# Optimization experiments

Measured on AMD Instinct MI355X. Metric: run time of the kernel, lower is better.

The kernel has to match this reference:

```python
import jax, jax.numpy as jnp
import numpy as np
from jax import lax

B, H, W = 64, 40, 40
K = 24        # num_capsules == num_templates
TS = 11       # template_size
F = 16        # num_feature_maps
PI = 3.141592653589793


def setup_inputs() -> dict:
    key = jax.random.key(0)
    ks = jax.random.split(key, 12)
    def nrm(k, shape, s):
        return jax.random.normal(k, shape, dtype=jnp.float32) * s
    inp = {"x": jax.random.normal(ks[0], (B, 1, H, W), dtype=jnp.float32)}
    wshapes = [(K, 128, 1, 3, 3), (K, 128, 128, 3, 3), (K, 128, 128, 3, 3), (K, 128, 128, 3, 3), (K, F, 128, 1, 1)]
    for i, sh in enumerate(wshapes):
        fan_in = sh[2] * sh[3] * sh[4]
        inp["w%d" % (i + 1)] = nrm(ks[1 + i], sh, (2.0 / fan_in) ** 0.5)
        inp["b%d" % (i + 1)] = nrm(ks[6 + i], (K, sh[1]), 0.1)
    inp["templates"] = jax.random.normal(ks[11], (K, TS, TS), dtype=jnp.float32)
    return inp


def _capsule(x, w1, b1, w2, b2, w3, b3, w4, b4, w5, b5):
    # one part-capsule conv stack; x: [B,1,H,W]
    def cv(h, w, b, s):
        y = lax.conv_general_dilated(h, w, (s, s), 'VALID', dimension_numbers=('NCHW', 'OIHW', 'NCHW'))
        return y + b[None, :, None, None]
    h = jax.nn.relu(cv(x, w1, b1, 2))
    h = jax.nn.relu(cv(h, w2, b2, 2))
    h = jax.nn.relu(cv(h, w3, b3, 1))
    h = jax.nn.relu(cv(h, w4, b4, 1))
    return cv(h, w5, b5, 1)  # [B,F,5,5]


def _warp(templates, pose, Ho, Wo):
    # Batched replacement for the per-sample PIL affine + resize round-trip.
    # templates: [T,TS,TS]; pose: [B,T,6] = (angle_deg, tx, ty, scale, shear_x_deg, shear_y_deg)
    T_ = templates.shape[0]
    ang = jnp.deg2rad(pose[..., 0])
    tx, ty = pose[..., 1], pose[..., 2]
    sc = jnp.maximum(pose[..., 3], 1e-2)  # guard against scale==0 from ReLU
    shx = jnp.deg2rad(pose[..., 4])
    shy = jnp.deg2rad(pose[..., 5])
    cx = cy = (TS - 1) * 0.5
    # torchvision _get_inverse_affine_matrix
    a = jnp.cos(ang - shy) / jnp.cos(shy)
    b = -jnp.cos(ang - shy) * jnp.tan(shx) / jnp.cos(shy) - jnp.sin(ang)
    c = jnp.sin(ang - shy) / jnp.cos(shy)
    d = -jnp.sin(ang - shy) * jnp.tan(shx) / jnp.cos(shy) + jnp.cos(ang)
    m0 = d / sc; m1 = -b / sc; m3 = -c / sc; m4 = a / sc
    m2 = m0 * (-cx - tx) + m1 * (-cy - ty) + cx
    m5 = m3 * (-cx - tx) + m4 * (-cy - ty) + cy
    # output grid in template pixel coords (fuses the bilinear resize TS->HoxWo)
    gy = (jnp.arange(Ho, dtype=jnp.float32) + 0.5) * TS / Ho - 0.5
    gx = (jnp.arange(Wo, dtype=jnp.float32) + 0.5) * TS / Wo - 0.5
    yo, xo = jnp.meshgrid(gy, gx, indexing='ij')  # [Ho,Wo]
    xin = m0[..., None, None] * xo + m1[..., None, None] * yo + m2[..., None, None]  # [B,T,Ho,Wo]
    yin = m3[..., None, None] * xo + m4[..., None, None] * yo + m5[..., None, None]
    x0 = jnp.floor(xin); y0 = jnp.floor(yin)
    wx = xin - x0; wy = yin - y0
    x0i = x0.astype(jnp.int32); y0i = y0.astype(jnp.int32)
    tidx = jnp.arange(T_)[None, :, None, None]
    def tap(yi, xi):
        valid = (xi >= 0) & (xi < TS) & (yi >= 0) & (yi < TS)
        v = templates[tidx, jnp.clip(yi, 0, TS - 1), jnp.clip(xi, 0, TS - 1)]
        return jnp.where(valid, v, 0.0)
    return (tap(y0i, x0i) * (1 - wx) * (1 - wy) + tap(y0i, x0i + 1) * wx * (1 - wy)
            + tap(y0i + 1, x0i) * (1 - wx) * wy + tap(y0i + 1, x0i + 1) * wx * wy)


def reference(x, w1, b1, w2, b2, w3, b3, w4, b4, w5, b5, templates):
    out = jax.vmap(_capsule, in_axes=(None,) + (0,) * 10)(x, w1, b1, w2, b2, w3, b3, w4, b4, w5, b5)  # [K,B,F,5,5]
    # torch Softmax(2) on [B,Hc,Wc] attention map = softmax over each row (last axis)
    att = jax.nn.softmax(out[:, :, -1], axis=-1)                       # [K,B,5,5]
    pooled = jnp.sum(out[:, :, :-1] * att[:, :, None], axis=(-2, -1))  # [K,B,F-1]
    p = pooled.transpose(1, 0, 2)                                      # [B,K,F-1]
    x_m = jax.nn.relu(p[:, :, :6])
    d_m = jax.nn.sigmoid(p[:, :, 6:7])
    c_z = jax.nn.relu(p[:, :, 7:])
    Bn = x.shape[0]
    # PIL round-trip in the original detaches gradients from templates/poses
    tt = lax.stop_gradient(_warp(templates, x_m, H, W))                # [B,K,H,W]
    mix = jax.nn.softmax(d_m * tt.reshape(Bn, K, -1), axis=-1).reshape(Bn, K, H, W)
    std = jnp.std(x.reshape(Bn, -1), axis=-1, ddof=1).reshape(Bn, 1, 1, 1)
    mult = 1.0 / jnp.sqrt(std * 2.0 * PI)
    pw = -1.0 / (2.0 * std * std)
    g = mult * jnp.exp((lax.stop_gradient(x) - tt) ** 2 * pw)          # [B,K,H,W]
    ll = jnp.mean(jnp.sum(jnp.log(jnp.sum(g * mix, axis=1)), axis=(-2, -1)))
    tflat = jnp.broadcast_to(lax.stop_gradient(templates).reshape(1, K, TS * TS), (Bn, K, TS * TS))
    input_ocae = jnp.concatenate([lax.stop_gradient(d_m), lax.stop_gradient(x_m), tflat, c_z], axis=-1)
    return ll, input_ocae, lax.stop_gradient(x_m), lax.stop_gradient(d_m)
```

## Files before the change

### kernel.cpp

```cpp
#include <hip/hip_runtime.h>
#include <math.h>

#define TPB 256

typedef __attribute__((ext_vector_type(8))) short s16x8;
typedef __attribute__((ext_vector_type(4))) short s16x4;
typedef __attribute__((ext_vector_type(4))) float f32x4;
typedef unsigned int u32;

constexpr int Bn = 64, Kc = 24, TSz = 11;
constexpr int NBK = Bn * Kc;
constexpr int P2 = 81, P3 = 49, P4 = 25;

constexpr size_t SZW_B    = (size_t)Kc * 36 * 4096 * 2;
constexpr size_t OFFB_W2  = 0;
constexpr size_t OFFB_W3  = OFFB_W2 + SZW_B;
constexpr size_t OFFB_W4  = OFFB_W3 + SZW_B;
constexpr size_t OFFB_POSE= OFFB_W4 + SZW_B;
constexpr size_t OFFB_DMV = OFFB_POSE + (size_t)NBK * 6 * 4;
constexpr size_t OFFB_TT  = OFFB_DMV + (size_t)NBK * 4;
constexpr size_t OFFB_ST  = OFFB_TT + (size_t)NBK * 1600 * 4;
constexpr size_t OFFB_MXS = OFFB_ST + 512;
constexpr size_t OFFB_PART= OFFB_MXS + (size_t)NBK * 2 * 4;

constexpr int OUT_OC = 1;
constexpr int OUT_XM = 1 + NBK * 136;
constexpr int OUT_DM = OUT_XM + NBK * 6;

__device__ __forceinline__ ushort f2b(float f) {
    union { float f; unsigned u; } c; c.f = f;
    unsigned r = c.u + 0x7fffu + ((c.u >> 16) & 1u);
    return (ushort)(r >> 16);
}
__device__ __forceinline__ float b2f(ushort h) {
    union { unsigned u; float f; } c; c.u = ((unsigned)h) << 16; return c.f;
}

__device__ __forceinline__ float blockReduceSum(float v) {
    __shared__ float red[4];
    __syncthreads();
#pragma unroll
    for (int o = 32; o > 0; o >>= 1) v += __shfl_down(v, o, 64);
    int lane = threadIdx.x & 63, wv = threadIdx.x >> 6;
    if (lane == 0) red[wv] = v;
    __syncthreads();
    return red[0] + red[1] + red[2] + red[3];
}

__device__ __forceinline__ float blockReduceMax(float v) {
    __shared__ float redm[4];
    __syncthreads();
#pragma unroll
    for (int o = 32; o > 0; o >>= 1) v = fmaxf(v, __shfl_down(v, o, 64));
    int lane = threadIdx.x & 63, wv = threadIdx.x >> 6;
    if (lane == 0) redm[wv] = v;
    __syncthreads();
    return fmaxf(fmaxf(redm[0], redm[1]), fmaxf(redm[2], redm[3]));
}

__global__ __launch_bounds__(TPB) void prep_k(
    const float* __restrict__ w2, const float* __restrict__ w3,
    const float* __restrict__ w4, const float* __restrict__ x,
    ushort* __restrict__ wt2, ushort* __restrict__ wt3,
    ushort* __restrict__ wt4, float* __restrict__ st) {
    const int bid = blockIdx.x;
    if (bid < 9216) {
        __shared__ float ld[1152];
        const float* w = bid < 3072 ? w2 : (bid < 6144 ? w3 : w4);
        ushort* wt = bid < 3072 ? wt2 : (bid < 6144 ? wt3 : wt4);
        const int kb = bid & 3071;
        const int kk = (bid % 3072) >> 7, cout = bid & 127;
        (void)kb;
        const float* src = w + (size_t)(kk * 128 + cout) * 1152;
        for (int i = threadIdx.x; i < 1152; i += TPB) ld[i] = src[i];
        __syncthreads();
        const int n = cout >> 4, l16 = cout & 15;
        for (int e = threadIdx.x; e < 1152; e += TPB) {
            int cb = e / 288, r = e - cb * 288, tap = r >> 5, c32 = r & 31;
            int cin = cb * 32 + c32;
            size_t d = (size_t)((kk * 4 + cb) * 9 + tap) * 4096
                     + n * 512 + (c32 >> 3) * 128 + l16 * 8 + (c32 & 7);
            wt[d] = f2b(ld[cin * 9 + tap]);
        }
    } else {
        const int b = bid - 9216;
        const float* xb = x + b * 1600;
        float s = 0.f, s2 = 0.f;
        for (int p = threadIdx.x; p < 1600; p += TPB) {
            float v = xb[p];
            s += v; s2 += v * v;
        }
        s = blockReduceSum(s);
        s2 = blockReduceSum(s2);
        if (threadIdx.x == 0) {
            float mean = s / 1600.f;
            float var = (s2 - 1600.f * mean * mean) / 1599.f;
            float sd = sqrtf(var);
            st[b * 2] = rsqrtf(sd * 6.283185307179586f);
            st[b * 2 + 1] = -1.f / (2.f * sd * sd);
        }
    }
}

__global__ __launch_bounds__(256) void convall_k(
    const float* __restrict__ x, const float* __restrict__ w1,
    const float* __restrict__ b1,
    const ushort* __restrict__ wt2, const float* __restrict__ b2,
    const ushort* __restrict__ wt3, const float* __restrict__ b3,
    const ushort* __restrict__ wt4, const float* __restrict__ b4,
    const float* __restrict__ w5, const float* __restrict__ b5,
    const float* __restrict__ tpl,
    float* __restrict__ pose, float* __restrict__ dmv,
    float* __restrict__ out) {
    __shared__ __align__(16) ushort pool[17680];
    float*  xs  = (float*)pool;
    ushort* As  = pool + 3200;
    ushort* h2L = pool;
    ushort* h3L = pool + 11016;
    float*  h4s = (float*)pool;
    float*  outs= (float*)(pool + 6400);
    float*  atts= (float*)(pool + 7200);
    float*  pooled = (float*)(pool + 7264);

    const int bi = blockIdx.x;
    const int xcd = bi & 7, jj = bi >> 3;
    const int k = xcd * 3 + jj % 3, b = jj / 3;
    const int bkL = b * 24 + k;
    const int tid = threadIdx.x;
    const int w = tid >> 6, l = tid & 63, l16 = l & 15, g = l >> 4;
    const int mgrp = w >> 1, ngrp = w & 1;

    {
        constexpr int OP = 81, STR = 40;
        const int sl = tid & 7, p0 = tid >> 3;
        const ushort* wb = wt2 + (size_t)k * 36 * 4096 + ngrp * 2048 + g * 128 + l16 * 8;
        const float* w1k = w1 + (size_t)k * 1152;
        const float* b1k = b1 + k * 128;

        for (int i = tid; i < 400; i += 256)
            ((f32x4*)xs)[i] = ((const f32x4*)(x + b * 1600))[i];

        s16x8 breg[3][4];
#pragma unroll
        for (int n = 0; n < 4; ++n) breg[0][n] = *(const s16x8*)(wb + n * 512);
#pragma unroll
        for (int n = 0; n < 4; ++n) breg[1][n] = *(const s16x8*)(wb + 4096 + n * 512);

        f32x4 acc[3][4];
#pragma unroll
        for (int m = 0; m < 3; ++m)
#pragma unroll
            for (int n = 0; n < 4; ++n) acc[m][n] = (f32x4)0.f;

        int ibase[3];
#pragma unroll
        for (int m = 0; m < 3; ++m) {
            int row = (mgrp * 3 + m) * 16 + l16;
            row = row < OP ? row : OP - 1;
            int oy = row / 9, ox = row - oy * 9;
            ibase[m] = oy * 38 + ox * 2;
        }

        float wq[36], bq[4];
        auto conv1_slab = [&]() {
            for (int p = p0; p < 361; p += 32) {
                int py = p / 19, px = p - py * 19;
                const float* xb = xs + py * 80 + px * 2;
                float xt[9];
#pragma unroll
                for (int dy = 0; dy < 3; ++dy)
#pragma unroll
                    for (int dx = 0; dx < 3; ++dx) xt[dy * 3 + dx] = xb[dy * 40 + dx];
                s16x4 v;
#pragma unroll
                for (int j2 = 0; j2 < 4; ++j2) {
                    float s2 = bq[j2];
#pragma unroll
                    for (int t9 = 0; t9 < 9; ++t9) s2 += wq[j2 * 9 + t9] * xt[t9];
                    v[j2] = (short)f2b(fmaxf(s2, 0.f));
                }
                *(s16x4*)(As + p * STR + 8 * ((sl >> 1) ^ ((p >> 3) & 1)) + (sl & 1) * 4) = v;
            }
        };

        {
            const float* wsrc = w1k + (sl * 4) * 9;
#pragma unroll
            for (int i2 = 0; i2 < 9; ++i2) ((f32x4*)wq)[i2] = ((const f32x4*)wsrc)[i2];
            *(f32x4*)bq = *(const f32x4*)(b1k + sl * 4);
        }
        __syncthreads();
        conv1_slab();
        __syncthreads();

#pragma unroll
        for (int cb = 0; cb < 4; ++cb) {
            if (cb < 3) {
                const float* wsrc = w1k + ((cb + 1) * 32 + sl * 4) * 9;
#pragma unroll
                for (int i2 = 0; i2 < 9; ++i2) ((f32x4*)wq)[i2] = ((const f32x4*)wsrc)[i2];
                *(f32x4*)bq = *(const f32x4*)(b1k + (cb + 1) * 32 + sl * 4);
            }
#pragma unroll
            for (int tap = 0; tap < 9; ++tap) {
                const int it = cb * 9 + tap;
                if (it + 2 < 36) {
                    const ushort* src = wb + (size_t)(it + 2) * 4096;
#pragma unroll
                    for (int n = 0; n < 4; ++n)
                        breg[(it + 2) % 3][n] = *(const s16x8*)(src + n * 512);
                }
                const int ioff = (tap / 3) * 19 + (tap % 3);
                s16x8 a[3];
#pragma unroll
                for (int m = 0; m < 3; ++m) {
                    int ip = ibase[m] + ioff;
                    a[m] = *(const s16x8*)(As + ip * STR + 8 * (g ^ ((ip >> 3) & 1)));
                }
#pragma unroll
                for (int n = 0; n < 4; ++n)
#pragma unroll
                    for (int m = 0; m < 3; ++m)
                        acc[m][n] = __builtin_amdgcn_mfma_f32_16x16x32_bf16(a[m], breg[it % 3][n], acc[m][n], 0, 0, 0);
            }
            if (cb < 3) {
                __syncthreads();
                conv1_slab();
                __syncthreads();
            }
        }
        __syncthreads();
#pragma unroll
        for (int n = 0; n < 4; ++n) {
            int cout = (ngrp * 4 + n) * 16 + l16;
            float bv = b2[k * 128 + cout];
#pragma unroll
            for (int m = 0; m < 3; ++m)
#pragma unroll
                for (int r = 0; r < 4; ++r) {
                    int row = (mgrp * 3 + m) * 16 + g * 4 + r;
                    if (row < OP)
                        h2L[row * 136 + cout] = f2b(fmaxf(acc[m][n][r] + bv, 0.f));
                }
        }
    }
    __syncthreads();

    {
        constexpr int OP = 49;
        const ushort* wb = wt3 + (size_t)k * 36 * 4096 + ngrp * 2048 + g * 128 + l16 * 8;
        s16x8 breg[2][4];
#pragma unroll
        for (int n = 0; n < 4; ++n) breg[0][n] = *(const s16x8*)(wb + n * 512);
#pragma unroll
        for (int n = 0; n < 4; ++n) breg[1][n] = *(const s16x8*)(wb + 4096 + n * 512);

        f32x4 acc[2][4];
#pragma unroll
        for (int m = 0; m < 2; ++m)
#pragma unroll
            for (int n = 0; n < 4; ++n) acc[m][n] = (f32x4)0.f;

        int ibase[2];
#pragma unroll
        for (int m = 0; m < 2; ++m) {
            int row = (mgrp * 2 + m) * 16 + l16;
            row = row < OP ? row : OP - 1;
            int oy = row / 7, ox = row - oy * 7;
            ibase[m] = oy * 9 + ox;
        }
#pragma unroll
        for (int cb = 0; cb < 4; ++cb)
#pragma unroll
            for (int tap = 0; tap < 9; ++tap) {
                const int it = cb * 9 + tap;
                if (it + 1 < 36) {
                    const ushort* src = wb + (size_t)(it + 1) * 4096;
#pragma unroll
                    for (int n = 0; n < 4; ++n)
                        breg[(it + 1) & 1][n] = *(const s16x8*)(src + n * 512);
                }
                const int ioff = (tap / 3) * 9 + (tap % 3);
                s16x8 a[2];
#pragma unroll
                for (int m = 0; m < 2; ++m)
                    a[m] = *(const s16x8*)(h2L + (ibase[m] + ioff) * 136 + cb * 32 + g * 8);
#pragma unroll
                for (int n = 0; n < 4; ++n)
#pragma unroll
                    for (int m = 0; m < 2; ++m)
                        acc[m][n] = __builtin_amdgcn_mfma_f32_16x16x32_bf16(a[m], breg[it & 1][n], acc[m][n], 0, 0, 0);
            }
#pragma unroll
        for (int n = 0; n < 4; ++n) {
            int cout = (ngrp * 4 + n) * 16 + l16;
            float bv = b3[k * 128 + cout];
#pragma unroll
            for (int m = 0; m < 2; ++m)
#pragma unroll
                for (int r = 0; r < 4; ++r) {
                    int row = (mgrp * 2 + m) * 16 + g * 4 + r;
                    if (row < OP)
                        h3L[row * 136 + cout] = f2b(fmaxf(acc[m][n][r] + bv, 0.f));
                }
        }
    }
    __syncthreads();

    {
        constexpr int OP = 25;
        const ushort* wb = wt4 + (size_t)k * 36 * 4096 + ngrp * 2048 + g * 128 + l16 * 8;
        s16x8 breg[2][4];
#pragma unroll
        for (int n = 0; n < 4; ++n) breg[0][n] = *(const s16x8*)(wb + n * 512);
#pragma unroll
        for (int n = 0; n < 4; ++n) breg[1][n] = *(const s16x8*)(wb + 4096 + n * 512);

        f32x4 acc[4];
#pragma unroll
        for (int n = 0; n < 4; ++n) acc[n] = (f32x4)0.f;

        int ibase;
        {
            int row = mgrp * 16 + l16;
            row = row < OP ? row : OP - 1;
            int oy = row / 5, ox = row - oy * 5;
            ibase = oy * 7 + ox;
        }
#pragma unroll
        for (int cb = 0; cb < 4; ++cb)
#pragma unroll
            for (int tap = 0; tap < 9; ++tap) {
                const int it = cb * 9 + tap;
                if (it + 1 < 36) {
                    const ushort* src = wb + (size_t)(it + 1) * 4096;
#pragma unroll
                    for (int n = 0; n < 4; ++n)
                        breg[(it + 1) & 1][n] = *(const s16x8*)(src + n * 512);
                }
                const int ioff = (tap / 3) * 7 + (tap % 3);
                s16x8 a = *(const s16x8*)(h3L + (ibase + ioff) * 136 + cb * 32 + g * 8);
#pragma unroll
                for (int n = 0; n < 4; ++n)
                    acc[n] = __builtin_amdgcn_mfma_f32_16x16x32_bf16(a, breg[it & 1][n], acc[n], 0, 0, 0);
            }
#pragma unroll
        for (int n = 0; n < 4; ++n) {
            int cout = (ngrp * 4 + n) * 16 + l16;
            float bv = b4[k * 128 + cout];
#pragma unroll
            for (int r = 0; r < 4; ++r) {
                int row = mgrp * 16 + g * 4 + r;
                if (row < OP)
                    h4s[cout * 25 + row] = fmaxf(acc[n][r] + bv, 0.f);
            }
        }
    }
    __syncthreads();

    for (int t = tid; t < 400; t += 256) {
        int f = t / 25, pix = t - f * 25;
        const float* wp = w5 + (size_t)(k * 16 + f) * 128;
        float s = b5[k * 16 + f];
        for (int c = 0; c < 128; ++c) s += wp[c] * h4s[c * 25 + pix];
        outs[t] = s;
    }
    __syncthreads();
    if (tid < 25) {
        int y5 = tid / 5;
        const float* row = outs + 15 * 25 + y5 * 5;
        float mx = row[0];
#pragma unroll
        for (int j = 1; j < 5; ++j) mx = fmaxf(mx, row[j]);
        float ssum = 0.f;
#pragma unroll
        for (int j = 0; j < 5; ++j) ssum += expf(row[j] - mx);
        atts[tid] = expf(outs[15 * 25 + tid] - mx) / ssum;
    }
    __syncthreads();
    if (tid < 15) {
        float s = 0.f;
        const float* row = outs + tid * 25;
#pragma unroll
        for (int p = 0; p < 25; ++p) s += row[p] * atts[p];
        pooled[tid] = s;
    }
    __syncthreads();
    float* oc = out + OUT_OC + (size_t)bkL * 136;
    if (tid < 6) {
        float v = fmaxf(pooled[tid], 0.f);
        pose[bkL * 6 + tid] = v;
        oc[1 + tid] = v;
        out[OUT_XM + bkL * 6 + tid] = v;
    } else if (tid == 6) {
        float d = 1.f / (1.f + expf(-pooled[6]));
        dmv[bkL] = d;
        oc[0] = d;
        out[OUT_DM + bkL] = d;
    } else if (tid >= 7 && tid < 15) {
        oc[128 + tid - 7] = fmaxf(pooled[tid], 0.f);
    }
    for (int t = tid; t < 121; t += 256) oc[7 + t] = tpl[k * 121 + t];
}

__device__ __forceinline__ float tapf(const float* tp, int y, int x) {
    bool valid = (x >= 0) && (x < TSz) && (y >= 0) && (y < TSz);
    int yc = min(max(y, 0), TSz - 1), xc = min(max(x, 0), TSz - 1);
    float v = tp[yc * TSz + xc];
    return valid ? v : 0.f;
}

__global__ __launch_bounds__(TPB) void warp_mix_k(const float* __restrict__ pose,
                                                  const float* __restrict__ tpl,
                                                  const float* __restrict__ dmv,
                                                  float* __restrict__ tt,
                                                  float* __restrict__ mxs) {
    __shared__ float tp[121];
    const int bk = blockIdx.x, k = bk % Kc;
    for (int i = threadIdx.x; i < 121; i += TPB) tp[i] = tpl[k * 121 + i];
    const float* ps = pose + bk * 6;
    const float D2R = 0.017453292519943295f;
    float ang = ps[0] * D2R, tx = ps[1], ty = ps[2];
    float sc = fmaxf(ps[3], 1e-2f);
    float shx = ps[4] * D2R, shy = ps[5] * D2R;
    float cams = cosf(ang - shy), sams = sinf(ang - shy);
    float cshy = cosf(shy), tshx = tanf(shx);
    float av = cams / cshy;
    float bv = -cams * tshx / cshy - sinf(ang);
    float cv = sams / cshy;
    float dv = -sams * tshx / cshy + cosf(ang);
    float m0 = dv / sc, m1 = -bv / sc, m3 = -cv / sc, m4 = av / sc;
    float m2 = m0 * (-5.f - tx) + m1 * (-5.f - ty) + 5.f;
    float m5 = m3 * (-5.f - tx) + m4 * (-5.f - ty) + 5.f;
    __syncthreads();
    float* to = tt + (size_t)bk * 1600;
    float tvl[7];
#pragma unroll
    for (int r = 0; r < 7; ++r) {
        int p = threadIdx.x + r * TPB;
        float val = 0.f;
        if (p < 1600) {
            int i = p / 40, jx = p - (p / 40) * 40;
            float gx = (jx + 0.5f) * (11.f / 40.f) - 0.5f;
            float gy = (i + 0.5f) * (11.f / 40.f) - 0.5f;
            float xin = m0 * gx + m1 * gy + m2;
            float yin = m3 * gx + m4 * gy + m5;
            float x0 = floorf(xin), y0 = floorf(yin);
            float wx = xin - x0, wy = yin - y0;
            int x0i = (int)x0, y0i = (int)y0;
            float v00 = tapf(tp, y0i, x0i),     v01 = tapf(tp, y0i, x0i + 1);
            float v10 = tapf(tp, y0i + 1, x0i), v11 = tapf(tp, y0i + 1, x0i + 1);
            val = v00 * (1.f - wx) * (1.f - wy) + v01 * wx * (1.f - wy) +
                  v10 * (1.f - wx) * wy + v11 * wx * wy;
            to[p] = val;
        }
        tvl[r] = val;
    }
    const float dm = dmv[bk];
    float mx = -1e30f;
#pragma unroll
    for (int r = 0; r < 7; ++r) {
        int p = threadIdx.x + r * TPB;
        if (p < 1600) mx = fmaxf(mx, dm * tvl[r]);
    }
    mx = blockReduceMax(mx);
    float s = 0.f;
#pragma unroll
    for (int r = 0; r < 7; ++r) {
        int p = threadIdx.x + r * TPB;
        if (p < 1600) s += expf(dm * tvl[r] - mx);
    }
    s = blockReduceSum(s);
    if (threadIdx.x == 0) { mxs[bk * 2] = mx; mxs[bk * 2 + 1] = s; }
}

__global__ __launch_bounds__(TPB) void ll_k(const float* __restrict__ x,
                                            const float* __restrict__ tt,
                                            const float* __restrict__ dmv,
                                            const float* __restrict__ mxs,
                                            const float* __restrict__ st,
                                            float* __restrict__ part) {
    const int b = blockIdx.x, sp = blockIdx.y;
    __shared__ float dms[24], mxh[24], sih[24];
    if (threadIdx.x < 24) {
        int bk = b * 24 + threadIdx.x;
        dms[threadIdx.x] = dmv[bk];
        mxh[threadIdx.x] = mxs[bk * 2];
        sih[threadIdx.x] = 1.f / mxs[bk * 2 + 1];
    }
    __syncthreads();
    const float mult = st[b * 2], pw = st[b * 2 + 1];
    const float* xb = x + b * 1600;
    const float* tb = tt + (size_t)b * 24 * 1600;
    float acc = 0.f;
    int p = sp * 200 + threadIdx.x;
    if (threadIdx.x < 200) {
        float xv = xb[p];
        float ssum = 0.f;
        for (int k = 0; k < 24; ++k) {
            float tv = tb[(size_t)k * 1600 + p];
            float dd = xv - tv;
            float g = mult * expf(dd * dd * pw);
            float mixv = expf(dms[k] * tv - mxh[k]) * sih[k];
            ssum += g * mixv;
        }
        acc = logf(ssum);
    }
    acc = blockReduceSum(acc);
    if (threadIdx.x == 0) part[b * 8 + sp] = acc;
}

__global__ void fin_k(const float* __restrict__ part, float* __restrict__ out) {
    float v = 0.f;
#pragma unroll
    for (int q = 0; q < 8; ++q) v += part[threadIdx.x * 8 + q];
#pragma unroll
    for (int o = 32; o > 0; o >>= 1) v += __shfl_down(v, o, 64);
    if (threadIdx.x == 0) out[0] = v * (1.f / 64.f);
}

extern "C" void kernel_launch(void* const* d_in, const int* in_sizes, int n_in,
                              void* d_out, int out_size, void* d_ws, size_t ws_size,
                              hipStream_t stream) {
    const float* x   = (const float*)d_in[0];
    const float* w1  = (const float*)d_in[1];
    const float* b1  = (const float*)d_in[2];
    const float* w2  = (const float*)d_in[3];
    const float* b2  = (const float*)d_in[4];
    const float* w3  = (const float*)d_in[5];
    const float* b3  = (const float*)d_in[6];
    const float* w4  = (const float*)d_in[7];
    const float* b4  = (const float*)d_in[8];
    const float* w5  = (const float*)d_in[9];
    const float* b5  = (const float*)d_in[10];
    const float* tpl = (const float*)d_in[11];
    float* out = (float*)d_out;
    char* W = (char*)d_ws;

    ushort* wt2 = (ushort*)(W + OFFB_W2);
    ushort* wt3 = (ushort*)(W + OFFB_W3);
    ushort* wt4 = (ushort*)(W + OFFB_W4);
    float*  pose = (float*)(W + OFFB_POSE);
    float*  dmv  = (float*)(W + OFFB_DMV);
    float*  ttb  = (float*)(W + OFFB_TT);
    float*  stv  = (float*)(W + OFFB_ST);
    float*  mxs  = (float*)(W + OFFB_MXS);
    float*  part = (float*)(W + OFFB_PART);

    prep_k<<<3 * 3072 + Bn, TPB, 0, stream>>>(w2, w3, w4, x, wt2, wt3, wt4, stv);
    convall_k<<<NBK, 256, 0, stream>>>(x, w1, b1, wt2, b2, wt3, b3, wt4, b4,
                                       w5, b5, tpl, pose, dmv, out);
    warp_mix_k<<<NBK, TPB, 0, stream>>>(pose, tpl, dmv, ttb, mxs);
    ll_k<<<dim3(Bn, 8), TPB, 0, stream>>>(x, ttb, dmv, mxs, stv, part);
    fin_k<<<1, 64, 0, stream>>>(part, out);
}
```

Before: 203.5 us.

## Fuse template warp and softmax stats into conv kernel; shrink weight prefetch ring

Moves the affine template warp and the per-(b,k) softmax max/sum reduction into the tail of the conv kernel, computing pose directly from pooled values in shared memory. This removes one kernel launch and the pose buffer round trip through global memory. It also reduces the bf16 weight register prefetch from triple to double buffering and loads conv1 weights inside the slab lambda. The cost is a longer conv kernel tail and possibly less latency hiding for weight loads.

After: 204.6 us. No clear change (+0.5%).

```diff
diff --git a/kernel.cpp b/kernel.cpp
--- a/kernel.cpp
+++ b/kernel.cpp
@@ -10,14 +10,12 @@
 
 constexpr int Bn = 64, Kc = 24, TSz = 11;
 constexpr int NBK = Bn * Kc;
-constexpr int P2 = 81, P3 = 49, P4 = 25;
 
 constexpr size_t SZW_B    = (size_t)Kc * 36 * 4096 * 2;
 constexpr size_t OFFB_W2  = 0;
 constexpr size_t OFFB_W3  = OFFB_W2 + SZW_B;
 constexpr size_t OFFB_W4  = OFFB_W3 + SZW_B;
-constexpr size_t OFFB_POSE= OFFB_W4 + SZW_B;
-constexpr size_t OFFB_DMV = OFFB_POSE + (size_t)NBK * 6 * 4;
+constexpr size_t OFFB_DMV = OFFB_W4 + SZW_B;
 constexpr size_t OFFB_TT  = OFFB_DMV + (size_t)NBK * 4;
 constexpr size_t OFFB_ST  = OFFB_TT + (size_t)NBK * 1600 * 4;
 constexpr size_t OFFB_MXS = OFFB_ST + 512;
@@ -68,9 +66,7 @@
         __shared__ float ld[1152];
         const float* w = bid < 3072 ? w2 : (bid < 6144 ? w3 : w4);
         ushort* wt = bid < 3072 ? wt2 : (bid < 6144 ? wt3 : wt4);
-        const int kb = bid & 3071;
         const int kk = (bid % 3072) >> 7, cout = bid & 127;
-        (void)kb;
         const float* src = w + (size_t)(kk * 128 + cout) * 1152;
         for (int i = threadIdx.x; i < 1152; i += TPB) ld[i] = src[i];
         __syncthreads();
@@ -110,8 +106,8 @@
     const ushort* __restrict__ wt4, const float* __restrict__ b4,
     const float* __restrict__ w5, const float* __restrict__ b5,
     const float* __restrict__ tpl,
-    float* __restrict__ pose, float* __restrict__ dmv,
-    float* __restrict__ out) {
+    float* __restrict__ dmv, float* __restrict__ tt,
+    float* __restrict__ mxs, float* __restrict__ out) {
     __shared__ __align__(16) ushort pool[17680];
     float*  xs  = (float*)pool;
     ushort* As  = pool + 3200;
@@ -121,6 +117,7 @@
     float*  outs= (float*)(pool + 6400);
     float*  atts= (float*)(pool + 7200);
     float*  pooled = (float*)(pool + 7264);
+    float*  tp  = (float*)(pool + 7400);
 
     const int bi = blockIdx.x;
     const int xcd = bi & 7, jj = bi >> 3;
@@ -140,7 +137,7 @@
         for (int i = tid; i < 400; i += 256)
             ((f32x4*)xs)[i] = ((const f32x4*)(x + b * 1600))[i];
 
-        s16x8 breg[3][4];
+        s16x8 breg[2][4];
 #pragma unroll
         for (int n = 0; n < 4; ++n) breg[0][n] = *(const s16x8*)(wb + n * 512);
 #pragma unroll
@@ -161,8 +158,12 @@
             ibase[m] = oy * 38 + ox * 2;
         }
 
-        float wq[36], bq[4];
-        auto conv1_slab = [&]() {
+        auto conv1_slab = [&](int cb) {
+            float wq[36], bq[4];
+            const float* wsrc = w1k + (cb * 32 + sl * 4) * 9;
+#pragma unroll
+            for (int i2 = 0; i2 < 9; ++i2) ((f32x4*)wq)[i2] = ((const f32x4*)wsrc)[i2];
+            *(f32x4*)bq = *(const f32x4*)(b1k + cb * 32 + sl * 4);
             for (int p = p0; p < 361; p += 32) {
                 int py = p / 19, px = p - py * 19;
                 const float* xb = xs + py * 80 + px * 2;
@@ -183,32 +184,20 @@
             }
         };
 
-        {
-            const float* wsrc = w1k + (sl * 4) * 9;
-#pragma unroll
-            for (int i2 = 0; i2 < 9; ++i2) ((f32x4*)wq)[i2] = ((const f32x4*)wsrc)[i2];
-            *(f32x4*)bq = *(const f32x4*)(b1k + sl * 4);
-        }
         __syncthreads();
-        conv1_slab();
+        conv1_slab(0);
         __syncthreads();
 
 #pragma unroll
         for (int cb = 0; cb < 4; ++cb) {
-            if (cb < 3) {
-                const float* wsrc = w1k + ((cb + 1) * 32 + sl * 4) * 9;
-#pragma unroll
-                for (int i2 = 0; i2 < 9; ++i2) ((f32x4*)wq)[i2] = ((const f32x4*)wsrc)[i2];
-                *(f32x4*)bq = *(const f32x4*)(b1k + (cb + 1) * 32 + sl * 4);
-            }
 #pragma unroll
             for (int tap = 0; tap < 9; ++tap) {
                 const int it = cb * 9 + tap;
-                if (it + 2 < 36) {
-                    const ushort* src = wb + (size_t)(it + 2) * 4096;
+                if (it + 1 < 36) {
+                    const ushort* src = wb + (size_t)(it + 1) * 4096;
 #pragma unroll
                     for (int n = 0; n < 4; ++n)
-                        breg[(it + 2) % 3][n] = *(const s16x8*)(src + n * 512);
+                        breg[(it + 1) & 1][n] = *(const s16x8*)(src + n * 512);
                 }
                 const int ioff = (tap / 3) * 19 + (tap % 3);
                 s16x8 a[3];
@@ -221,11 +210,11 @@
                 for (int n = 0; n < 4; ++n)
 #pragma unroll
                     for (int m = 0; m < 3; ++m)
-                        acc[m][n] = __builtin_amdgcn_mfma_f32_16x16x32_bf16(a[m], breg[it % 3][n], acc[m][n], 0, 0, 0);
+                        acc[m][n] = __builtin_amdgcn_mfma_f32_16x16x32_bf16(a[m], breg[it & 1][n], acc[m][n], 0, 0, 0);
             }
             if (cb < 3) {
                 __syncthreads();
-                conv1_slab();
+                conv1_slab(cb + 1);
                 __syncthreads();
             }
         }
@@ -389,7 +378,6 @@
     float* oc = out + OUT_OC + (size_t)bkL * 136;
     if (tid < 6) {
         float v = fmaxf(pooled[tid], 0.f);
-        pose[bkL * 6 + tid] = v;
         oc[1 + tid] = v;
         out[OUT_XM + bkL * 6 + tid] = v;
     } else if (tid == 6) {
@@ -401,77 +389,71 @@
         oc[128 + tid - 7] = fmaxf(pooled[tid], 0.f);
     }
     for (int t = tid; t < 121; t += 256) oc[7 + t] = tpl[k * 121 + t];
-}
-
-__device__ __forceinline__ float tapf(const float* tp, int y, int x) {
-    bool valid = (x >= 0) && (x < TSz) && (y >= 0) && (y < TSz);
-    int yc = min(max(y, 0), TSz - 1), xc = min(max(x, 0), TSz - 1);
-    float v = tp[yc * TSz + xc];
-    return valid ? v : 0.f;
-}
-
-__global__ __launch_bounds__(TPB) void warp_mix_k(const float* __restrict__ pose,
-                                                  const float* __restrict__ tpl,
-                                                  const float* __restrict__ dmv,
-                                                  float* __restrict__ tt,
-                                                  float* __restrict__ mxs) {
-    __shared__ float tp[121];
-    const int bk = blockIdx.x, k = bk % Kc;
-    for (int i = threadIdx.x; i < 121; i += TPB) tp[i] = tpl[k * 121 + i];
-    const float* ps = pose + bk * 6;
-    const float D2R = 0.017453292519943295f;
-    float ang = ps[0] * D2R, tx = ps[1], ty = ps[2];
-    float sc = fmaxf(ps[3], 1e-2f);
-    float shx = ps[4] * D2R, shy = ps[5] * D2R;
-    float cams = cosf(ang - shy), sams = sinf(ang - shy);
-    float cshy = cosf(shy), tshx = tanf(shx);
-    float av = cams / cshy;
-    float bv = -cams * tshx / cshy - sinf(ang);
-    float cv = sams / cshy;
-    float dv = -sams * tshx / cshy + cosf(ang);
-    float m0 = dv / sc, m1 = -bv / sc, m3 = -cv / sc, m4 = av / sc;
-    float m2 = m0 * (-5.f - tx) + m1 * (-5.f - ty) + 5.f;
-    float m5 = m3 * (-5.f - tx) + m4 * (-5.f - ty) + 5.f;
-    __syncthreads();
-    float* to = tt + (size_t)bk * 1600;
-    float tvl[7];
-#pragma unroll
-    for (int r = 0; r < 7; ++r) {
-        int p = threadIdx.x + r * TPB;
-        float val = 0.f;
-        if (p < 1600) {
-            int i = p / 40, jx = p - (p / 40) * 40;
-            float gx = (jx + 0.5f) * (11.f / 40.f) - 0.5f;
-            float gy = (i + 0.5f) * (11.f / 40.f) - 0.5f;
-            float xin = m0 * gx + m1 * gy + m2;
-            float yin = m3 * gx + m4 * gy + m5;
-            float x0 = floorf(xin), y0 = floorf(yin);
-            float wx = xin - x0, wy = yin - y0;
-            int x0i = (int)x0, y0i = (int)y0;
-            float v00 = tapf(tp, y0i, x0i),     v01 = tapf(tp, y0i, x0i + 1);
-            float v10 = tapf(tp, y0i + 1, x0i), v11 = tapf(tp, y0i + 1, x0i + 1);
-            val = v00 * (1.f - wx) * (1.f - wy) + v01 * wx * (1.f - wy) +
-                  v10 * (1.f - wx) * wy + v11 * wx * wy;
-            to[p] = val;
-        }
-        tvl[r] = val;
-    }
-    const float dm = dmv[bk];
-    float mx = -1e30f;
-#pragma unroll
-    for (int r = 0; r < 7; ++r) {
-        int p = threadIdx.x + r * TPB;
-        if (p < 1600) mx = fmaxf(mx, dm * tvl[r]);
-    }
-    mx = blockReduceMax(mx);
-    float s = 0.f;
-#pragma unroll
-    for (int r = 0; r < 7; ++r) {
-        int p = threadIdx.x + r * TPB;
-        if (p < 1600) s += expf(dm * tvl[r] - mx);
-    }
-    s = blockReduceSum(s);
-    if (threadIdx.x == 0) { mxs[bk * 2] = mx; mxs[bk * 2 + 1] = s; }
+
+    for (int i = tid; i < 121; i += 256) tp[i] = tpl[k * 121 + i];
+    {
+        const float D2R = 0.017453292519943295f;
+        float ang = fmaxf(pooled[0], 0.f) * D2R;
+        float txp = fmaxf(pooled[1], 0.f), typ = fmaxf(pooled[2], 0.f);
+        float sc  = fmaxf(fmaxf(pooled[3], 0.f), 1e-2f);
+        float shx = fmaxf(pooled[4], 0.f) * D2R;
+        float shy = fmaxf(pooled[5], 0.f) * D2R;
+        float dm  = 1.f / (1.f + expf(-pooled[6]));
+        float cams = cosf(ang - shy), sams = sinf(ang - shy);
+        float cshy = cosf(shy), tshx = tanf(shx);
+        float av = cams / cshy;
+        float bv = -cams * tshx / cshy - sinf(ang);
+        float cv = sams / cshy;
+        float dv = -sams * tshx / cshy + cosf(ang);
+        float m0 = dv / sc, m1 = -bv / sc, m3 = -cv / sc, m4 = av / sc;
+        float m2 = m0 * (-5.f - txp) + m1 * (-5.f - typ) + 5.f;
+        float m5 = m3 * (-5.f - txp) + m4 * (-5.f - typ) + 5.f;
+        __syncthreads();
+        float* to = tt + (size_t)bkL * 1600;
+        float tvl[7];
+#pragma unroll
+        for (int r = 0; r < 7; ++r) {
+            int p = tid + r * 256;
+            float val = 0.f;
+            if (p < 1600) {
+                int i = p / 40, jx = p - (p / 40) * 40;
+                float gx = (jx + 0.5f) * (11.f / 40.f) - 0.5f;
+                float gy = (i + 0.5f) * (11.f / 40.f) - 0.5f;
+                float xin = m0 * gx + m1 * gy + m2;
+                float yin = m3 * gx + m4 * gy + m5;
+                float x0 = floorf(xin), y0 = floorf(yin);
+                float wx = xin - x0, wy = yin - y0;
+                int x0i = (int)x0, y0i = (int)y0;
+                auto tapf = [&](int yy, int xx) -> float {
+                    bool valid = (xx >= 0) && (xx < TSz) && (yy >= 0) && (yy < TSz);
+                    int yc = min(max(yy, 0), TSz - 1), xc = min(max(xx, 0), TSz - 1);
+                    float v = tp[yc * TSz + xc];
+                    return valid ? v : 0.f;
+                };
+                float v00 = tapf(y0i, x0i),     v01 = tapf(y0i, x0i + 1);
+                float v10 = tapf(y0i + 1, x0i), v11 = tapf(y0i + 1, x0i + 1);
+                val = v00 * (1.f - wx) * (1.f - wy) + v01 * wx * (1.f - wy) +
+                      v10 * (1.f - wx) * wy + v11 * wx * wy;
+                to[p] = val;
+            }
+            tvl[r] = val;
+        }
+        float mx = -1e30f;
+#pragma unroll
+        for (int r = 0; r < 7; ++r) {
+            int p = tid + r * 256;
+            if (p < 1600) mx = fmaxf(mx, dm * tvl[r]);
+        }
+        mx = blockReduceMax(mx);
+        float s = 0.f;
+#pragma unroll
+        for (int r = 0; r < 7; ++r) {
+            int p = tid + r * 256;
+            if (p < 1600) s += expf(dm * tvl[r] - mx);
+        }
+        s = blockReduceSum(s);
+        if (tid == 0) { mxs[bkL * 2] = mx; mxs[bkL * 2 + 1] = s; }
+    }
 }
 
 __global__ __launch_bounds__(TPB) void ll_k(const float* __restrict__ x,
@@ -540,7 +522,6 @@
     ushort* wt2 = (ushort*)(W + OFFB_W2);
     ushort* wt3 = (ushort*)(W + OFFB_W3);
     ushort* wt4 = (ushort*)(W + OFFB_W4);
-    float*  pose = (float*)(W + OFFB_POSE);
     float*  dmv  = (float*)(W + OFFB_DMV);
     float*  ttb  = (float*)(W + OFFB_TT);
     float*  stv  = (float*)(W + OFFB_ST);
@@ -549,8 +530,7 @@
 
     prep_k<<<3 * 3072 + Bn, TPB, 0, stream>>>(w2, w3, w4, x, wt2, wt3, wt4, stv);
     convall_k<<<NBK, 256, 0, stream>>>(x, w1, b1, wt2, b2, wt3, b3, wt4, b4,
-                                       w5, b5, tpl, pose, dmv, out);
-    warp_mix_k<<<NBK, TPB, 0, stream>>>(pose, tpl, dmv, ttb, mxs);
+                                       w5, b5, tpl, dmv, ttb, mxs, out);
     ll_k<<<dim3(Bn, 8), TPB, 0, stream>>>(x, ttb, dmv, mxs, stv, part);
     fin_k<<<1, 64, 0, stream>>>(part, out);
 }
```
